# Kernel tuning notes

Hardware: AMD Instinct MI355X
Metric: run time of the kernel (lower is better)

## Reference

```python
import jax, jax.numpy as jnp
import numpy as np

U, I, D, OUT = 8192, 16384, 64, 64

def setup_inputs() -> dict:
    key = jax.random.key(0)
    k1, k2, k3, k4 = jax.random.split(key, 4)
    user_emb = jax.random.normal(k1, (U, D), dtype=jnp.float32)
    item_emb = jax.random.normal(k2, (I, D), dtype=jnp.float32)
    attention_weight = jax.random.normal(k3, (D, OUT), dtype=jnp.float32) * (1.0 / np.sqrt(D))
    adj_matrix = jax.random.randint(k4, (U, I), 0, 2, dtype=jnp.int32)
    return {"user_emb": user_emb, "item_emb": item_emb,
            "attention_weight": attention_weight, "adj_matrix": adj_matrix}

def reference(user_emb, item_emb, attention_weight, adj_matrix):
    # score[u,i] = <user_emb[u], item_emb[i]>  (torch.inner)
    score = jnp.einsum('ud,id->ui', user_emb, item_emb)
    # mask non-edges to 0 (NOT -inf, faithful to torch.where(adj>0, score, 0))
    score = jnp.where(adj_matrix > 0, score, 0.0)
    score = jax.nn.softmax(score, axis=1)
    # flag == True path: aggregate items into users, then project
    output = score @ item_emb          # [U, D]
    output = output @ attention_weight  # [U, OUT]
    return output
```

## Files before the change

### kernel.cpp

```cpp
#include <hip/hip_runtime.h>
#include <hip/hip_bf16.h>
#include <math.h>

#define U_N   8192
#define I_N   16384
#define D_N   64
#define OUT_N 64
#define BN    32
#define BM    128
#define NCH   8
#define ITERS 64
#define VN_ST 72
#define VT_ST 40

typedef _Float16 half8  __attribute__((ext_vector_type(8)));
typedef short    bf16x8 __attribute__((ext_vector_type(8)));
typedef short    bf16x4 __attribute__((ext_vector_type(4)));
typedef float    f32x4  __attribute__((ext_vector_type(4)));
typedef int      int4v  __attribute__((ext_vector_type(4)));

static __device__ __forceinline__ unsigned short f2bf(float f) {
    union { __hip_bfloat16 h; unsigned short u; } cv;
    cv.h = __float2bfloat16(f);
    return cv.u;
}
static __device__ __forceinline__ float fast_exp2(float x) {
#if __has_builtin(__builtin_amdgcn_exp2f)
    return __builtin_amdgcn_exp2f(x);
#else
    return __expf(x * 0.6931471805599453f);
#endif
}
static __device__ __forceinline__ bf16x4 pack4(float a, float b, float c2, float d) {
    union { unsigned u[2]; bf16x4 h; } x;
#if __has_builtin(__builtin_amdgcn_perm)
    x.u[0] = __builtin_amdgcn_perm(__float_as_uint(b), __float_as_uint(a), 0x07060302u);
    x.u[1] = __builtin_amdgcn_perm(__float_as_uint(d), __float_as_uint(c2), 0x07060302u);
#else
    x.u[0] = (__float_as_uint(b) & 0xffff0000u) | (__float_as_uint(a) >> 16);
    x.u[1] = (__float_as_uint(d) & 0xffff0000u) | (__float_as_uint(c2) >> 16);
#endif
    return x.h;
}
static __device__ __forceinline__ void bar() {
    asm volatile("s_waitcnt lgkmcnt(0)\n\ts_barrier" ::: "memory");
}
static __device__ __forceinline__ f32x4 pv_mfma(bf16x4 a, bf16x4 b, f32x4 c) {
#if __has_builtin(__builtin_amdgcn_mfma_f32_16x16x16bf16_1k)
    return __builtin_amdgcn_mfma_f32_16x16x16bf16_1k(a, b, c, 0, 0, 0);
#else
    f32x4 d;
    asm volatile("v_mfma_f32_16x16x16_bf16 %0, %1, %2, %3"
                 : "=v"(d) : "v"(a), "v"(b), "v"(c));
    return d;
#endif
}

__global__ __launch_bounds__(256)
void prep_items(const float* __restrict__ item,
                _Float16* __restrict__ itemH,
                unsigned short* __restrict__ itemTt)
{
    const int tid = blockIdx.x * 256 + threadIdx.x;
    const int i   = tid >> 2;
    const int g   = tid & 3;
    const float* src = item + (size_t)i * D_N + g * 16;
    f32x4 v0 = *(const f32x4*)(src);
    f32x4 v1 = *(const f32x4*)(src + 4);
    f32x4 v2 = *(const f32x4*)(src + 8);
    f32x4 v3 = *(const f32x4*)(src + 12);

    half8 h0, h1;
    #pragma unroll
    for (int k = 0; k < 4; ++k) {
        h0[k] = (_Float16)v0[k]; h0[4 + k] = (_Float16)v1[k];
        h1[k] = (_Float16)v2[k]; h1[4 + k] = (_Float16)v3[k];
    }
    *(half8*)&itemH[(size_t)i * D_N + g * 16]     = h0;
    *(half8*)&itemH[(size_t)i * D_N + g * 16 + 8] = h1;

    const int il    = i & 31;
    const int islot = 8 * ((il & 15) >> 2) + ((il >> 4) << 2) + (il & 3);
    unsigned short* dst = itemTt + (size_t)(i >> 5) * (D_N * 32) + (size_t)(g * 16) * 32 + islot;
    #pragma unroll
    for (int k = 0; k < 4; ++k) {
        dst[(4 * 0 + k) * 32] = f2bf(v0[k]);
        dst[(4 * 1 + k) * 32] = f2bf(v1[k]);
        dst[(4 * 2 + k) * 32] = f2bf(v2[k]);
        dst[(4 * 3 + k) * 32] = f2bf(v3[k]);
    }
}

#define DECL_SET(S) \
    int4v adj##S##a0, adj##S##b0, adj##S##a1, adj##S##b1; \
    half8 vn##S; bf16x8 vt##S;

#define LOAD_ADJ(S, tidx) do { \
    const size_t o_ = (size_t)(tidx) * BN; \
    adj##S##a0 = *(const int4v*)&adjq0[o_];      \
    adj##S##b0 = *(const int4v*)&adjq0[o_ + 16]; \
    adj##S##a1 = *(const int4v*)&adjq1[o_];      \
    adj##S##b1 = *(const int4v*)&adjq1[o_ + 16]; \
} while (0)

#define LOAD_TILE(S, tidx) do { \
    const size_t o_ = (size_t)(tidx) * BN; \
    vn##S = *(const half8*)&itemH[(ibase0 + o_ + (t >> 3)) * D_N + (t & 7) * 8]; \
    vt##S = *(const bf16x8*)&itemTt[((ibase0 + o_) >> 5) * (D_N * 32) \
                                    + (size_t)(t >> 2) * 32 + (t & 3) * 8]; \
} while (0)

#define COMMIT(S, bufw) do { \
    *(half8*)&Vn[bufw][(t >> 3) * VN_ST + (t & 7) * 8] = vn##S; \
    *(bf16x8*)&Vt[bufw][(t >> 2) * VT_ST + (t & 3) * 8] = vt##S; \
} while (0)

#define COMPUTE_REST(S, bufr) do { \
    half8 a00 = *(const half8*)&Vn[bufr][(c)      * VN_ST      + q * 8]; \
    half8 a01 = *(const half8*)&Vn[bufr][(c)      * VN_ST + 32 + q * 8]; \
    half8 a10 = *(const half8*)&Vn[bufr][(16 + c) * VN_ST      + q * 8]; \
    half8 a11 = *(const half8*)&Vn[bufr][(16 + c) * VN_ST + 32 + q * 8]; \
    bf16x8 w0 = *(const bf16x8*)&Vt[bufr][(c)      * VT_ST + 8 * q]; \
    bf16x8 w1 = *(const bf16x8*)&Vt[bufr][(16 + c) * VT_ST + 8 * q]; \
    bf16x8 w2 = *(const bf16x8*)&Vt[bufr][(32 + c) * VT_ST + 8 * q]; \
    bf16x8 w3 = *(const bf16x8*)&Vt[bufr][(48 + c) * VT_ST + 8 * q]; \
    f32x4 T0 = (f32x4){0.f,0.f,0.f,0.f}; \
    f32x4 T1 = T0, T2 = T0, T3 = T0; \
    T0 = __builtin_amdgcn_mfma_f32_16x16x32_f16(a00, ufrag0, T0, 0, 0, 0); \
    T2 = __builtin_amdgcn_mfma_f32_16x16x32_f16(a00, ufrag2, T2, 0, 0, 0); \
    T0 = __builtin_amdgcn_mfma_f32_16x16x32_f16(a01, ufrag1, T0, 0, 0, 0); \
    T2 = __builtin_amdgcn_mfma_f32_16x16x32_f16(a01, ufrag3, T2, 0, 0, 0); \
    T1 = __builtin_amdgcn_mfma_f32_16x16x32_f16(a10, ufrag0, T1, 0, 0, 0); \
    T3 = __builtin_amdgcn_mfma_f32_16x16x32_f16(a10, ufrag2, T3, 0, 0, 0); \
    T1 = __builtin_amdgcn_mfma_f32_16x16x32_f16(a11, ufrag1, T1, 0, 0, 0); \
    T3 = __builtin_amdgcn_mfma_f32_16x16x32_f16(a11, ufrag3, T3, 0, 0, 0); \
    const float e0_ = fast_exp2((adj##S##a0[0] != 0) ? T0[0] : 0.0f); \
    const float e1_ = fast_exp2((adj##S##a0[1] != 0) ? T0[1] : 0.0f); \
    const float e2_ = fast_exp2((adj##S##a0[2] != 0) ? T0[2] : 0.0f); \
    const float e3_ = fast_exp2((adj##S##a0[3] != 0) ? T0[3] : 0.0f); \
    const float f0_ = fast_exp2((adj##S##b0[0] != 0) ? T1[0] : 0.0f); \
    const float f1_ = fast_exp2((adj##S##b0[1] != 0) ? T1[1] : 0.0f); \
    const float f2_ = fast_exp2((adj##S##b0[2] != 0) ? T1[2] : 0.0f); \
    const float f3_ = fast_exp2((adj##S##b0[3] != 0) ? T1[3] : 0.0f); \
    const float g0_ = fast_exp2((adj##S##a1[0] != 0) ? T2[0] : 0.0f); \
    const float g1_ = fast_exp2((adj##S##a1[1] != 0) ? T2[1] : 0.0f); \
    const float g2_ = fast_exp2((adj##S##a1[2] != 0) ? T2[2] : 0.0f); \
    const float g3_ = fast_exp2((adj##S##a1[3] != 0) ? T2[3] : 0.0f); \
    const float h0_ = fast_exp2((adj##S##b1[0] != 0) ? T3[0] : 0.0f); \
    const float h1_ = fast_exp2((adj##S##b1[1] != 0) ? T3[1] : 0.0f); \
    const float h2_ = fast_exp2((adj##S##b1[2] != 0) ? T3[2] : 0.0f); \
    const float h3_ = fast_exp2((adj##S##b1[3] != 0) ? T3[3] : 0.0f); \
    lc0 += ((e0_ + e1_) + (e2_ + e3_)) + ((f0_ + f1_) + (f2_ + f3_)); \
    lc1 += ((g0_ + g1_) + (g2_ + g3_)) + ((h0_ + h1_) + (h2_ + h3_)); \
    bf16x4 p0 = pack4(e0_, e1_, e2_, e3_); \
    bf16x4 p1 = pack4(f0_, f1_, f2_, f3_); \
    bf16x4 p2 = pack4(g0_, g1_, g2_, g3_); \
    bf16x4 p3 = pack4(h0_, h1_, h2_, h3_); \
    bf16x4 lo0 = __builtin_shufflevector(w0, w0, 0, 1, 2, 3); \
    bf16x4 hi0 = __builtin_shufflevector(w0, w0, 4, 5, 6, 7); \
    bf16x4 lo1 = __builtin_shufflevector(w1, w1, 0, 1, 2, 3); \
    bf16x4 hi1 = __builtin_shufflevector(w1, w1, 4, 5, 6, 7); \
    bf16x4 lo2 = __builtin_shufflevector(w2, w2, 0, 1, 2, 3); \
    bf16x4 hi2 = __builtin_shufflevector(w2, w2, 4, 5, 6, 7); \
    bf16x4 lo3 = __builtin_shufflevector(w3, w3, 0, 1, 2, 3); \
    bf16x4 hi3 = __builtin_shufflevector(w3, w3, 4, 5, 6, 7); \
    O0 = pv_mfma(p0, lo0, O0);  O4 = pv_mfma(p2, lo0, O4); \
    O0 = pv_mfma(p1, hi0, O0);  O4 = pv_mfma(p3, hi0, O4); \
    O1 = pv_mfma(p0, lo1, O1);  O5 = pv_mfma(p2, lo1, O5); \
    O1 = pv_mfma(p1, hi1, O1);  O5 = pv_mfma(p3, hi1, O5); \
    O2 = pv_mfma(p0, lo2, O2);  O6 = pv_mfma(p2, lo2, O6); \
    O2 = pv_mfma(p1, hi2, O2);  O6 = pv_mfma(p3, hi2, O6); \
    O3 = pv_mfma(p0, lo3, O3);  O7 = pv_mfma(p2, lo3, O7); \
    O3 = pv_mfma(p1, hi3, O3);  O7 = pv_mfma(p3, hi3, O7); \
} while (0)

__global__ __launch_bounds__(256, 3)
void atten_main(const float* __restrict__ user_emb,
                const _Float16* __restrict__ itemH,
                const unsigned short* __restrict__ itemTt,
                const int*   __restrict__ adj,
                float* __restrict__ wsO,
                float* __restrict__ wsL)
{
    __shared__ _Float16 Vn[2][BN * VN_ST];
    __shared__ short    Vt[2][D_N * VT_ST];

    const int ch   = blockIdx.x;
    const int ub   = blockIdx.y;
    const int t    = threadIdx.x;
    const int w    = t >> 6;
    const int lane = t & 63;
    const int c    = lane & 15;
    const int q    = lane >> 4;

    const int    urow0  = ub * BM + w * 16;
    const size_t ibase0 = (size_t)ch * (I_N / NCH);

    half8 ufrag0, ufrag1, ufrag2, ufrag3;
    {
        const float s = 1.44269504088896f;
        const float* up0 = user_emb + (size_t)(urow0 + c) * D_N + q * 8;
        const float* up1 = up0 + (size_t)64 * D_N;
        f32x4 a0 = *(const f32x4*)(up0);
        f32x4 b0 = *(const f32x4*)(up0 + 4);
        f32x4 a1 = *(const f32x4*)(up0 + 32);
        f32x4 b1 = *(const f32x4*)(up0 + 36);
        f32x4 a2 = *(const f32x4*)(up1);
        f32x4 b2 = *(const f32x4*)(up1 + 4);
        f32x4 a3 = *(const f32x4*)(up1 + 32);
        f32x4 b3 = *(const f32x4*)(up1 + 36);
        #pragma unroll
        for (int j = 0; j < 4; ++j) {
            ufrag0[j] = (_Float16)(a0[j] * s); ufrag0[4 + j] = (_Float16)(b0[j] * s);
            ufrag1[j] = (_Float16)(a1[j] * s); ufrag1[4 + j] = (_Float16)(b1[j] * s);
            ufrag2[j] = (_Float16)(a2[j] * s); ufrag2[4 + j] = (_Float16)(b2[j] * s);
            ufrag3[j] = (_Float16)(a3[j] * s); ufrag3[4 + j] = (_Float16)(b3[j] * s);
        }
    }

    f32x4 O0 = (f32x4){0.f,0.f,0.f,0.f};
    f32x4 O1 = O0, O2 = O0, O3 = O0, O4 = O0, O5 = O0, O6 = O0, O7 = O0;
    float lc0 = 0.f, lc1 = 0.f;

    const int* adjq0 = adj + (size_t)(urow0 + c) * I_N + ibase0 + 4 * q;
    const int* adjq1 = adjq0 + (size_t)64 * I_N;

    DECL_SET(A)
    DECL_SET(B)

    LOAD_TILE(A, 0); LOAD_ADJ(A, 0);
    LOAD_TILE(B, 1); LOAD_ADJ(B, 1);
    COMMIT(A, 0);
    LOAD_TILE(A, 2);
    bar();

    for (int k = 0; k < ITERS; k += 2) {
        {
            COMMIT(B, 1);
            LOAD_TILE(B, (k + 3 < ITERS) ? k + 3 : ITERS - 1);
            COMPUTE_REST(A, 0);
            LOAD_ADJ(A, (k + 2 < ITERS) ? k + 2 : ITERS - 1);
            bar();
        }
        {
            COMMIT(A, 0);
            LOAD_TILE(A, (k + 4 < ITERS) ? k + 4 : ITERS - 1);
            COMPUTE_REST(B, 1);
            LOAD_ADJ(B, (k + 3 < ITERS) ? k + 3 : ITERS - 1);
            bar();
        }
    }

    lc0 += __shfl_xor(lc0, 16);
    lc0 += __shfl_xor(lc0, 32);
    lc1 += __shfl_xor(lc1, 16);
    lc1 += __shfl_xor(lc1, 32);

    {
        float* d0 = wsO + ((size_t)ch * U_N + urow0 + 4 * q + 0) * D_N;
        float* d1 = wsO + ((size_t)ch * U_N + urow0 + 4 * q + 1) * D_N;
        float* d2 = wsO + ((size_t)ch * U_N + urow0 + 4 * q + 2) * D_N;
        float* d3 = wsO + ((size_t)ch * U_N + urow0 + 4 * q + 3) * D_N;
        d0[c] = O0[0]; d0[16 + c] = O1[0]; d0[32 + c] = O2[0]; d0[48 + c] = O3[0];
        d1[c] = O0[1]; d1[16 + c] = O1[1]; d1[32 + c] = O2[1]; d1[48 + c] = O3[1];
        d2[c] = O0[2]; d2[16 + c] = O1[2]; d2[32 + c] = O2[2]; d2[48 + c] = O3[2];
        d3[c] = O0[3]; d3[16 + c] = O1[3]; d3[32 + c] = O2[3]; d3[48 + c] = O3[3];
        float* e0 = d0 + (size_t)64 * D_N;
        float* e1 = d1 + (size_t)64 * D_N;
        float* e2 = d2 + (size_t)64 * D_N;
        float* e3 = d3 + (size_t)64 * D_N;
        e0[c] = O4[0]; e0[16 + c] = O5[0]; e0[32 + c] = O6[0]; e0[48 + c] = O7[0];
        e1[c] = O4[1]; e1[16 + c] = O5[1]; e1[32 + c] = O6[1]; e1[48 + c] = O7[1];
        e2[c] = O4[2]; e2[16 + c] = O5[2]; e2[32 + c] = O6[2]; e2[48 + c] = O7[2];
        e3[c] = O4[3]; e3[16 + c] = O5[3]; e3[32 + c] = O6[3]; e3[48 + c] = O7[3];
    }
    if (q == 0) {
        wsL[(size_t)ch * U_N + urow0 + c]      = lc0;
        wsL[(size_t)ch * U_N + urow0 + 64 + c] = lc1;
    }
}

__global__ __launch_bounds__(256)
void atten_combine(const float* __restrict__ wsO,
                   const float* __restrict__ wsL,
                   const float* __restrict__ attw,
                   float* __restrict__ out,
                   int nch)
{
    __shared__ float inv[64];
    __shared__ float agg[64][68];
    __shared__ float Wl[64][68];

    const int t  = threadIdx.x;
    const int u0 = blockIdx.x * 64;

    {
        const int d = t >> 2, o0 = (t & 3) * 16;
        const float* src = attw + d * OUT_N + o0;
        #pragma unroll
        for (int j = 0; j < 4; ++j)
            *(f32x4*)&Wl[d][o0 + 4 * j] = *(const f32x4*)(src + 4 * j);
    }
    if (t < 64) {
        float L = 0.f;
        for (int cc = 0; cc < nch; ++cc) L += wsL[(size_t)cc * U_N + u0 + t];
        inv[t] = 1.0f / L;
    }
    __syncthreads();

    {
        const int ul = t >> 2, d0 = (t & 3) * 16;
        const int u = u0 + ul;
        f32x4 a4[4];
        #pragma unroll
        for (int j = 0; j < 4; ++j) a4[j] = (f32x4){0.f, 0.f, 0.f, 0.f};
        for (int cc = 0; cc < nch; ++cc) {
            const float* src = wsO + ((size_t)cc * U_N + u) * D_N + d0;
            #pragma unroll
            for (int j = 0; j < 4; ++j) a4[j] += *(const f32x4*)(src + 4 * j);
        }
        const float s = inv[ul];
        #pragma unroll
        for (int j = 0; j < 4; ++j)
            *(f32x4*)&agg[ul][d0 + 4 * j] = a4[j] * s;
    }
    __syncthreads();

    {
        const int ul = t >> 2, o0 = (t & 3) * 16;
        f32x4 acc[4];
        #pragma unroll
        for (int j = 0; j < 4; ++j) acc[j] = (f32x4){0.f, 0.f, 0.f, 0.f};
        for (int d = 0; d < 64; ++d) {
            const float av = agg[ul][d];
            #pragma unroll
            for (int j = 0; j < 4; ++j) {
                f32x4 wv = *(const f32x4*)&Wl[d][o0 + 4 * j];
                acc[j] += wv * av;
            }
        }
        float* dst = out + (size_t)(u0 + ul) * OUT_N + o0;
        #pragma unroll
        for (int j = 0; j < 4; ++j)
            *(f32x4*)(dst + 4 * j) = acc[j];
    }
}

extern "C" void kernel_launch(void* const* d_in, const int* in_sizes, int n_in,
                              void* d_out, int out_size, void* d_ws, size_t ws_size,
                              hipStream_t stream)
{
    const float* user_emb = (const float*)d_in[0];
    const float* item_emb = (const float*)d_in[1];
    const float* attw     = (const float*)d_in[2];
    const int*   adj      = (const int*)d_in[3];
    float* out = (float*)d_out;

    float*          wsO    = (float*)d_ws;
    float*          wsL    = wsO + (size_t)NCH * U_N * D_N;
    _Float16*       itemH  = (_Float16*)(wsL + (size_t)NCH * U_N);
    unsigned short* itemTt = (unsigned short*)(itemH + (size_t)I_N * D_N);

    prep_items<<<dim3(I_N * 4 / 256), 256, 0, stream>>>(item_emb, itemH, itemTt);
    atten_main<<<dim3(NCH, U_N / BM), 256, 0, stream>>>(user_emb, itemH, itemTt, adj,
                                                        wsO, wsL);
    atten_combine<<<dim3(U_N / 64), 256, 0, stream>>>(wsO, wsL, attw, out, NCH);
}
```

Baseline: 736.2 us.

## Give each wave private LDS tile buffers, drop block barriers, split items into more chunks

Each wave now loads the full item tile into its own private LDS double buffer, so the block-wide barriers between pipeline stages are removed. The item dimension is split into 32 chunks instead of 8, which raises grid size and shortens each block's loop. The cost is four times the global/L2 item traffic per block, four times the LDS footprint (occupancy hint lowered to 2), more register staging, and a larger combine workload. Without barriers, correct ordering of LDS reads and writes within a wave depends on wave-level execution and the compiler's waitcnt insertion.

```diff
diff --git a/kernel.cpp b/kernel.cpp
--- a/kernel.cpp
+++ b/kernel.cpp
@@ -7,9 +7,8 @@
 #define D_N   64
 #define OUT_N 64
 #define BN    32
-#define BM    128
-#define NCH   8
-#define ITERS 64
+#define NCH   32
+#define ITERS 16
 #define VN_ST 72
 #define VT_ST 40
 
@@ -41,9 +40,6 @@
     x.u[1] = (__float_as_uint(d) & 0xffff0000u) | (__float_as_uint(c2) >> 16);
 #endif
     return x.h;
-}
-static __device__ __forceinline__ void bar() {
-    asm volatile("s_waitcnt lgkmcnt(0)\n\ts_barrier" ::: "memory");
 }
 static __device__ __forceinline__ f32x4 pv_mfma(bf16x4 a, bf16x4 b, f32x4 c) {
 #if __has_builtin(__builtin_amdgcn_mfma_f32_16x16x16bf16_1k)
@@ -93,7 +89,8 @@
 
 #define DECL_SET(S) \
     int4v adj##S##a0, adj##S##b0, adj##S##a1, adj##S##b1; \
-    half8 vn##S; bf16x8 vt##S;
+    half8 vn##S##0, vn##S##1, vn##S##2, vn##S##3; \
+    bf16x8 vt##S##0, vt##S##1, vt##S##2, vt##S##3;
 
 #define LOAD_ADJ(S, tidx) do { \
     const size_t o_ = (size_t)(tidx) * BN; \
@@ -105,25 +102,42 @@
 
 #define LOAD_TILE(S, tidx) do { \
     const size_t o_ = (size_t)(tidx) * BN; \
-    vn##S = *(const half8*)&itemH[(ibase0 + o_ + (t >> 3)) * D_N + (t & 7) * 8]; \
-    vt##S = *(const bf16x8*)&itemTt[((ibase0 + o_) >> 5) * (D_N * 32) \
-                                    + (size_t)(t >> 2) * 32 + (t & 3) * 8]; \
+    const _Float16* hs_ = itemH + (ibase0 + o_) * D_N + 8 * lane; \
+    const unsigned short* ts_ = itemTt + ((ibase0 + o_) >> 5) * (D_N * 32) + 8 * lane; \
+    vn##S##0 = *(const half8*)&hs_[0];    \
+    vn##S##1 = *(const half8*)&hs_[512];  \
+    vn##S##2 = *(const half8*)&hs_[1024]; \
+    vn##S##3 = *(const half8*)&hs_[1536]; \
+    vt##S##0 = *(const bf16x8*)&ts_[0];    \
+    vt##S##1 = *(const bf16x8*)&ts_[512];  \
+    vt##S##2 = *(const bf16x8*)&ts_[1024]; \
+    vt##S##3 = *(const bf16x8*)&ts_[1536]; \
 } while (0)
 
 #define COMMIT(S, bufw) do { \
-    *(half8*)&Vn[bufw][(t >> 3) * VN_ST + (t & 7) * 8] = vn##S; \
-    *(bf16x8*)&Vt[bufw][(t >> 2) * VT_ST + (t & 3) * 8] = vt##S; \
+    _Float16* vw_ = &Vn[w][bufw][0]; \
+    short*    tw_ = &Vt[w][bufw][0]; \
+    *(half8*)&vw_[ni]        = vn##S##0; \
+    *(half8*)&vw_[ni + 576]  = vn##S##1; \
+    *(half8*)&vw_[ni + 1152] = vn##S##2; \
+    *(half8*)&vw_[ni + 1728] = vn##S##3; \
+    *(bf16x8*)&tw_[ti]        = vt##S##0; \
+    *(bf16x8*)&tw_[ti + 640]  = vt##S##1; \
+    *(bf16x8*)&tw_[ti + 1280] = vt##S##2; \
+    *(bf16x8*)&tw_[ti + 1920] = vt##S##3; \
 } while (0)
 
 #define COMPUTE_REST(S, bufr) do { \
-    half8 a00 = *(const half8*)&Vn[bufr][(c)      * VN_ST      + q * 8]; \
-    half8 a01 = *(const half8*)&Vn[bufr][(c)      * VN_ST + 32 + q * 8]; \
-    half8 a10 = *(const half8*)&Vn[bufr][(16 + c) * VN_ST      + q * 8]; \
-    half8 a11 = *(const half8*)&Vn[bufr][(16 + c) * VN_ST + 32 + q * 8]; \
-    bf16x8 w0 = *(const bf16x8*)&Vt[bufr][(c)      * VT_ST + 8 * q]; \
-    bf16x8 w1 = *(const bf16x8*)&Vt[bufr][(16 + c) * VT_ST + 8 * q]; \
-    bf16x8 w2 = *(const bf16x8*)&Vt[bufr][(32 + c) * VT_ST + 8 * q]; \
-    bf16x8 w3 = *(const bf16x8*)&Vt[bufr][(48 + c) * VT_ST + 8 * q]; \
+    const _Float16* vr_ = &Vn[w][bufr][0]; \
+    const short*    tr_ = &Vt[w][bufr][0]; \
+    half8 a00 = *(const half8*)&vr_[(c)      * VN_ST      + q * 8]; \
+    half8 a01 = *(const half8*)&vr_[(c)      * VN_ST + 32 + q * 8]; \
+    half8 a10 = *(const half8*)&vr_[(16 + c) * VN_ST      + q * 8]; \
+    half8 a11 = *(const half8*)&vr_[(16 + c) * VN_ST + 32 + q * 8]; \
+    bf16x8 w0 = *(const bf16x8*)&tr_[(c)      * VT_ST + 8 * q]; \
+    bf16x8 w1 = *(const bf16x8*)&tr_[(16 + c) * VT_ST + 8 * q]; \
+    bf16x8 w2 = *(const bf16x8*)&tr_[(32 + c) * VT_ST + 8 * q]; \
+    bf16x8 w3 = *(const bf16x8*)&tr_[(48 + c) * VT_ST + 8 * q]; \
     f32x4 T0 = (f32x4){0.f,0.f,0.f,0.f}; \
     f32x4 T1 = T0, T2 = T0, T3 = T0; \
     T0 = __builtin_amdgcn_mfma_f32_16x16x32_f16(a00, ufrag0, T0, 0, 0, 0); \
@@ -174,7 +188,7 @@
     O3 = pv_mfma(p1, hi3, O3);  O7 = pv_mfma(p3, hi3, O7); \
 } while (0)
 
-__global__ __launch_bounds__(256, 3)
+__global__ __launch_bounds__(256, 2)
 void atten_main(const float* __restrict__ user_emb,
                 const _Float16* __restrict__ itemH,
                 const unsigned short* __restrict__ itemTt,
@@ -182,8 +196,8 @@
                 float* __restrict__ wsO,
                 float* __restrict__ wsL)
 {
-    __shared__ _Float16 Vn[2][BN * VN_ST];
-    __shared__ short    Vt[2][D_N * VT_ST];
+    __shared__ _Float16 Vn[4][2][BN * VN_ST];
+    __shared__ short    Vt[4][2][D_N * VT_ST];
 
     const int ch   = blockIdx.x;
     const int ub   = blockIdx.y;
@@ -193,8 +207,11 @@
     const int c    = lane & 15;
     const int q    = lane >> 4;
 
-    const int    urow0  = ub * BM + w * 16;
+    const int    urow0  = ub * 128 + w * 16;
     const size_t ibase0 = (size_t)ch * (I_N / NCH);
+
+    const int ni = (lane >> 3) * VN_ST + (lane & 7) * 8;
+    const int ti = (lane >> 2) * VT_ST + (lane & 3) * 8;
 
     half8 ufrag0, ufrag1, ufrag2, ufrag3;
     {
@@ -232,7 +249,6 @@
     LOAD_TILE(B, 1); LOAD_ADJ(B, 1);
     COMMIT(A, 0);
     LOAD_TILE(A, 2);
-    bar();
 
     for (int k = 0; k < ITERS; k += 2) {
         {
@@ -240,14 +256,12 @@
             LOAD_TILE(B, (k + 3 < ITERS) ? k + 3 : ITERS - 1);
             COMPUTE_REST(A, 0);
             LOAD_ADJ(A, (k + 2 < ITERS) ? k + 2 : ITERS - 1);
-            bar();
         }
         {
             COMMIT(A, 0);
             LOAD_TILE(A, (k + 4 < ITERS) ? k + 4 : ITERS - 1);
             COMPUTE_REST(B, 1);
             LOAD_ADJ(B, (k + 3 < ITERS) ? k + 3 : ITERS - 1);
-            bar();
         }
     }
 
@@ -362,7 +376,7 @@
     unsigned short* itemTt = (unsigned short*)(itemH + (size_t)I_N * D_N);
 
     prep_items<<<dim3(I_N * 4 / 256), 256, 0, stream>>>(item_emb, itemH, itemTt);
-    atten_main<<<dim3(NCH, U_N / BM), 256, 0, stream>>>(user_emb, itemH, itemTt, adj,
-                                                        wsO, wsL);
+    atten_main<<<dim3(NCH, U_N / 128), 256, 0, stream>>>(user_emb, itemH, itemTt, adj,
+                                                         wsO, wsL);
     atten_combine<<<dim3(U_N / 64), 256, 0, stream>>>(wsO, wsL, attw, out, NCH);
 }
```

After: 756.8 us. +2.8%, slower.
